# Kernel optimization log

Measured on AMD Instinct MI355X. Metric: run time of the kernel, lower is better.

The kernel has to match this reference:

```python
import jax, jax.numpy as jnp
import numpy as np

NUM_ITER = 10
NUM_LAYER = 3
EMB_DIM = 128
ALPHA = 0.1
NUM_ATOM_FEATS = 9
ATOM_VOCAB = 119
N_NODES = 50000
N_EDGES = 800000


def setup_inputs() -> dict:
    key = jax.random.key(0)
    ks = jax.random.split(key, 5)
    x = jax.random.randint(ks[0], (N_NODES, NUM_ATOM_FEATS), 0, ATOM_VOCAB, dtype=jnp.int64 if jax.config.jax_enable_x64 else jnp.int32)
    edge_index = jax.random.randint(ks[1], (2, N_EDGES), 0, N_NODES, dtype=jnp.int32)
    scale = 1.0 / np.sqrt(EMB_DIM)
    atom_emb = jax.random.normal(ks[2], (NUM_ATOM_FEATS, ATOM_VOCAB, EMB_DIM), dtype=jnp.float32) * 0.1
    Ws = jax.random.normal(ks[3], (NUM_LAYER, EMB_DIM, EMB_DIM), dtype=jnp.float32) * scale
    bs = jax.random.normal(ks[4], (NUM_LAYER, EMB_DIM), dtype=jnp.float32) * 0.01
    return {"x": x, "edge_index": edge_index, "atom_emb": atom_emb, "Ws": Ws, "bs": bs}


def _forward(x, edge_index, atom_emb, Ws, bs):
    N = x.shape[0]
    # AtomEncoder: sum of per-feature-column embeddings -> [N, d]
    h = jax.vmap(lambda tbl, ids: tbl[ids], in_axes=(0, 1))(atom_emb, x).sum(axis=0)
    # MLP stack with ReLU on all but last layer
    L = Ws.shape[0]
    for l in range(L):
        h = h @ Ws[l] + bs[l]
        if l != L - 1:
            h = jax.nn.relu(h)
    # gcn_norm with self loops, unit edge weights (eval mode: no edge dropout)
    self_idx = jnp.arange(N, dtype=edge_index.dtype)
    src = jnp.concatenate([edge_index[0], self_idx])
    dst = jnp.concatenate([edge_index[1], self_idx])
    deg = jax.ops.segment_sum(jnp.ones(src.shape[0], dtype=h.dtype), dst, num_segments=N)
    dinv = jnp.where(deg > 0, jax.lax.rsqrt(jnp.maximum(deg, 1e-12)), 0.0)
    coef = (dinv[src] * dinv[dst])[:, None]  # [E+N, 1]
    h0 = h
    def body(i, h):
        agg = jax.ops.segment_sum(coef * h[src], dst, num_segments=N)
        return (1.0 - ALPHA) * agg + ALPHA * h0
    h = jax.lax.fori_loop(0, NUM_ITER, body, h)
    return h  # JK == 'last'


def reference(x, edge_index, atom_emb, Ws, bs):
    return _forward(x, edge_index, atom_emb, Ws, bs)
```

## Files before the change

kernel.cpp:

```cpp
#include <hip/hip_runtime.h>

#define N_NODES 50000
#define NPAD    50048
#define N_EDGES 800000
#define EMB 128
#define NFEAT 9
#define VOCAB 119
#define NITER 10
#define ALPHA 0.1f

typedef __attribute__((ext_vector_type(8))) short bf16x8;
typedef __attribute__((ext_vector_type(4))) float f32x4;


__device__ inline unsigned int f2bf1(float x) {
    union { float f; unsigned u; } v; v.f = x;
    unsigned r = v.u + 0x7fffu + ((v.u >> 16) & 1u);
    return r >> 16;
}
__device__ inline unsigned int f2bf2(float lo, float hi) {
    return f2bf1(lo) | (f2bf1(hi) << 16);
}
__device__ inline float bf2f_lo(unsigned u) {
    union { unsigned u; float f; } v; v.u = u << 16; return v.f;
}
__device__ inline float bf2f_hi(unsigned u) {
    union { unsigned u; float f; } v; v.u = u & 0xffff0000u; return v.f;
}

struct __attribute__((aligned(4))) i4 { int x, y, z, w; };


__global__ void k_zero(int* __restrict__ cnt) {
    int i = blockIdx.x * blockDim.x + threadIdx.x;
    if (i < N_NODES) cnt[i] = 0;
}

__global__ void k_count(const int* __restrict__ dst, int* __restrict__ cnt,
                        int* __restrict__ ord) {
    int e = blockIdx.x * blockDim.x + threadIdx.x;
    if (e < N_EDGES) ord[e] = atomicAdd(&cnt[dst[e]], 1);
}

__global__ void k_scan1(const int* __restrict__ cnt, int* __restrict__ rowptr,
                        int* __restrict__ bsum, float* __restrict__ dinv) {
    __shared__ int s[256];
    int t = threadIdx.x;
    int idx = blockIdx.x * 256 + t;
    int v = (idx < N_NODES) ? cnt[idx] : 0;
    if (idx < N_NODES) dinv[idx] = rsqrtf((float)(v + 1));
    s[t] = v; __syncthreads();
    for (int off = 1; off < 256; off <<= 1) {
        int add = (t >= off) ? s[t - off] : 0;
        __syncthreads();
        s[t] += add;
        __syncthreads();
    }
    if (idx < N_NODES) rowptr[idx] = s[t] - v;
    if (t == 255) bsum[blockIdx.x] = s[255];
}

__global__ void k_scan2(int* __restrict__ bsum, int nb) {
    __shared__ int s[256];
    int t = threadIdx.x;
    int v = (t < nb) ? bsum[t] : 0;
    s[t] = v; __syncthreads();
    for (int off = 1; off < 256; off <<= 1) {
        int add = (t >= off) ? s[t - off] : 0;
        __syncthreads();
        s[t] += add;
        __syncthreads();
    }
    if (t < nb) bsum[t] = s[t] - v;
}

__global__ void k_scan3(int* __restrict__ rowptr, const int* __restrict__ bsum) {
    int idx = blockIdx.x * 256 + threadIdx.x;
    if (idx < N_NODES) rowptr[idx] += bsum[blockIdx.x];
}

__global__ void k_fill(const int* __restrict__ src, const int* __restrict__ dst,
                       const int* __restrict__ ord, const int* __restrict__ rowptr,
                       int* __restrict__ csr_src) {
    int e = blockIdx.x * blockDim.x + threadIdx.x;
    if (e < N_EDGES) {
        csr_src[rowptr[dst[e]] + ord[e]] = src[e];
    }
}


__global__ void k_wprep(const float* __restrict__ W, ushort* __restrict__ WT) {
    int l = blockIdx.x >> 7;
    int n = blockIdx.x & 127;
    int k = threadIdx.x;
    WT[(l * 128 + n) * 128 + k] = (ushort)f2bf1(W[(l * 128 + k) * 128 + n]);
}


__global__ void k_encode(const int* __restrict__ x, const float* __restrict__ emb,
                         unsigned* __restrict__ hb) {
    int t = threadIdx.x;
    int sub = t >> 6;
    int dq = t & 63;
    int n = blockIdx.x * 4 + sub;
    const int* xr = x + n * NFEAT;
    float s0 = 0.f, s1 = 0.f;
#pragma unroll
    for (int f = 0; f < NFEAT; ++f) {
        const float2 e = *(const float2*)&emb[(f * VOCAB + xr[f]) * EMB + 2 * dq];
        s0 += e.x; s1 += e.y;
    }
    hb[n * 64 + dq] = f2bf2(s0, s1);
}


template <int RELU, int WQ>
__global__ __launch_bounds__(256) void k_mlp_mfma(
        const uint4* __restrict__ inb,
        uint4* __restrict__ outb,
        const uint4* __restrict__ WT4,
        const float* __restrict__ bias,
        const float* __restrict__ dinv,
        float* __restrict__ h0out,
        ushort* __restrict__ q0out,
        ushort* __restrict__ h0bout) {
    int t = threadIdx.x;
    int w = t >> 6;
    int l = t & 63;
    int lr = l & 15;
    int kg = l >> 4;
    int base = blockIdx.x * 64 + w * 16;
    union U { uint4 u; bf16x8 b; };

    int arow = base + lr;
    bf16x8 afrag[4];
#pragma unroll
    for (int kc = 0; kc < 4; ++kc) {
        U cu; cu.u = inb[arow * 16 + kc * 4 + kg];
        afrag[kc] = cu.b;
    }

    f32x4 acc[8];
#pragma unroll
    for (int nt = 0; nt < 8; ++nt) {
        float bv = bias[nt * 16 + lr];
        acc[nt] = (f32x4){bv, bv, bv, bv};
    }

#pragma unroll
    for (int kc = 0; kc < 4; ++kc) {
#pragma unroll
        for (int nt = 0; nt < 8; ++nt) {
            U cu; cu.u = WT4[(nt * 16 + lr) * 16 + kc * 4 + kg];
            acc[nt] = __builtin_amdgcn_mfma_f32_16x16x32_bf16(afrag[kc], cu.b,
                                                              acc[nt], 0, 0, 0);
        }
    }

    int orow = base + kg * 4;
    float dv[4];
    if (WQ) {
#pragma unroll
        for (int r = 0; r < 4; ++r) dv[r] = dinv[orow + r];
    }
#pragma unroll
    for (int nt = 0; nt < 8; ++nt) {
        int n = nt * 16 + lr;
#pragma unroll
        for (int r = 0; r < 4; ++r) {
            float val = acc[nt][r];
            if (RELU) val = fmaxf(val, 0.f);
            if (WQ) {
                h0out[(orow + r) * 128 + n] = val;
                q0out[(orow + r) * 128 + n] = (ushort)f2bf1(val * dv[r]);
                h0bout[(orow + r) * 128 + n] = (ushort)f2bf1(val);
            } else {
                ((ushort*)outb)[(orow + r) * 128 + n] = (ushort)f2bf1(val);
            }
        }
    }
}


#define ACC8(g) \
    a0 += bf2f_lo((g).x); a1 += bf2f_hi((g).x); \
    a2 += bf2f_lo((g).y); a3 += bf2f_hi((g).y); \
    a4 += bf2f_lo((g).z); a5 += bf2f_hi((g).z); \
    a6 += bf2f_lo((g).w); a7 += bf2f_hi((g).w);

#define SEL(iv) (pair == 0 ? (iv).x : pair == 1 ? (iv).y : pair == 2 ? (iv).z : (iv).w)

template <int LAST>
__global__ __launch_bounds__(256) void k_prop(const uint4* __restrict__ qin,
                                              const float4* __restrict__ h0,
                                              const uint4* __restrict__ h0b,
                                              void* __restrict__ outb,
                                              const int* __restrict__ rowptr,
                                              const int* __restrict__ cnt,
                                              const int* __restrict__ csr_src,
                                              const float* __restrict__ dinv) {
    int t = threadIdx.x;
    int lane = t & 63;
    int pair = lane >> 4;
    int dq = lane & 15;
    int v = blockIdx.x * 4 + (t >> 6);
    int start = __builtin_amdgcn_readfirstlane(rowptr[v]);
    int c = __builtin_amdgcn_readfirstlane(cnt[v]);
    const int* cs = csr_src + start;

    float dv = dinv[v];
    uint4 qv = qin[v * 16 + dq];
    float4 hlo, hhi; uint4 hvb;
    if (LAST) {
        hlo = h0[v * 32 + 2 * dq];
        hhi = h0[v * 32 + 2 * dq + 1];
    } else {
        hvb = h0b[v * 16 + dq];
    }

    float a0 = 0.f, a1 = 0.f, a2 = 0.f, a3 = 0.f;
    float a4 = 0.f, a5 = 0.f, a6 = 0.f, a7 = 0.f;
    int i = 0;
    for (; i + 32 <= c; i += 32) {
        i4 ia = *(const i4*)(cs + i);
        i4 ib = *(const i4*)(cs + i + 4);
        i4 ic = *(const i4*)(cs + i + 8);
        i4 id = *(const i4*)(cs + i + 12);
        i4 ie = *(const i4*)(cs + i + 16);
        i4 ifq = *(const i4*)(cs + i + 20);
        i4 ig = *(const i4*)(cs + i + 24);
        i4 ih = *(const i4*)(cs + i + 28);
        int s0 = SEL(ia), s1 = SEL(ib), s2 = SEL(ic), s3 = SEL(id);
        int s4 = SEL(ie), s5 = SEL(ifq), s6 = SEL(ig), s7 = SEL(ih);
        uint4 g0 = qin[s0 * 16 + dq];
        uint4 g1 = qin[s1 * 16 + dq];
        uint4 g2 = qin[s2 * 16 + dq];
        uint4 g3 = qin[s3 * 16 + dq];
        uint4 g4 = qin[s4 * 16 + dq];
        uint4 g5 = qin[s5 * 16 + dq];
        uint4 g6 = qin[s6 * 16 + dq];
        uint4 g7 = qin[s7 * 16 + dq];
        ACC8(g0); ACC8(g1); ACC8(g2); ACC8(g3);
        ACC8(g4); ACC8(g5); ACC8(g6); ACC8(g7);
    }
    for (; i + 8 <= c; i += 8) {
        i4 ia = *(const i4*)(cs + i);
        i4 ib = *(const i4*)(cs + i + 4);
        int s0 = SEL(ia), s1 = SEL(ib);
        uint4 g0 = qin[s0 * 16 + dq];
        uint4 g1 = qin[s1 * 16 + dq];
        ACC8(g0); ACC8(g1);
    }
    for (; i < c; i += 4) {
        int e = i + pair;
        if (e < c) {
            uint4 g = qin[cs[e] * 16 + dq];
            ACC8(g);
        }
    }
    a0 += __shfl_xor(a0, 16); a0 += __shfl_xor(a0, 32);
    a1 += __shfl_xor(a1, 16); a1 += __shfl_xor(a1, 32);
    a2 += __shfl_xor(a2, 16); a2 += __shfl_xor(a2, 32);
    a3 += __shfl_xor(a3, 16); a3 += __shfl_xor(a3, 32);
    a4 += __shfl_xor(a4, 16); a4 += __shfl_xor(a4, 32);
    a5 += __shfl_xor(a5, 16); a5 += __shfl_xor(a5, 32);
    a6 += __shfl_xor(a6, 16); a6 += __shfl_xor(a6, 32);
    a7 += __shfl_xor(a7, 16); a7 += __shfl_xor(a7, 32);

    float s0 = a0 + bf2f_lo(qv.x), s1 = a1 + bf2f_hi(qv.x);
    float s2 = a2 + bf2f_lo(qv.y), s3 = a3 + bf2f_hi(qv.y);
    float s4 = a4 + bf2f_lo(qv.z), s5 = a5 + bf2f_hi(qv.z);
    float s6 = a6 + bf2f_lo(qv.w), s7 = a7 + bf2f_hi(qv.w);
    const float K = 1.f - ALPHA;

    if (LAST) {
        float h_0 = K * dv * s0 + ALPHA * hlo.x;
        float h_1 = K * dv * s1 + ALPHA * hlo.y;
        float h_2 = K * dv * s2 + ALPHA * hlo.z;
        float h_3 = K * dv * s3 + ALPHA * hlo.w;
        float h_4 = K * dv * s4 + ALPHA * hhi.x;
        float h_5 = K * dv * s5 + ALPHA * hhi.y;
        float h_6 = K * dv * s6 + ALPHA * hhi.z;
        float h_7 = K * dv * s7 + ALPHA * hhi.w;
        if (pair < 2) {
            float4 wv = (pair == 0) ? make_float4(h_0, h_1, h_2, h_3)
                                    : make_float4(h_4, h_5, h_6, h_7);
            ((float4*)outb)[v * 32 + 2 * dq + pair] = wv;
        }
    } else {
        float h_0 = K * dv * s0 + ALPHA * bf2f_lo(hvb.x);
        float h_1 = K * dv * s1 + ALPHA * bf2f_hi(hvb.x);
        float h_2 = K * dv * s2 + ALPHA * bf2f_lo(hvb.y);
        float h_3 = K * dv * s3 + ALPHA * bf2f_hi(hvb.y);
        float h_4 = K * dv * s4 + ALPHA * bf2f_lo(hvb.z);
        float h_5 = K * dv * s5 + ALPHA * bf2f_hi(hvb.z);
        float h_6 = K * dv * s6 + ALPHA * bf2f_lo(hvb.w);
        float h_7 = K * dv * s7 + ALPHA * bf2f_hi(hvb.w);
        if (pair == 0) {
            uint4 wv;
            wv.x = f2bf2(h_0 * dv, h_1 * dv);
            wv.y = f2bf2(h_2 * dv, h_3 * dv);
            wv.z = f2bf2(h_4 * dv, h_5 * dv);
            wv.w = f2bf2(h_6 * dv, h_7 * dv);
            ((uint4*)outb)[v * 16 + dq] = wv;
        }
    }
}


extern "C" void kernel_launch(void* const* d_in, const int* in_sizes, int n_in,
                              void* d_out, int out_size, void* d_ws, size_t ws_size,
                              hipStream_t stream) {
    const int*   x    = (const int*)d_in[0];
    const int*   ei   = (const int*)d_in[1];
    const float* emb  = (const float*)d_in[2];
    const float* Ws   = (const float*)d_in[3];
    const float* bs   = (const float*)d_in[4];
    float* out = (float*)d_out;

    const int* src = ei;
    const int* dst = ei + N_EDGES;

    char* w = (char*)d_ws;
    size_t off = 0;
    auto alloc = [&](size_t bytes) {
        void* p = w + off;
        off += (bytes + 255) & ~(size_t)255;
        return p;
    };
    float*  h0      = (float*)alloc((size_t)NPAD * EMB * 4);
    void*   hb      = alloc((size_t)NPAD * EMB * 2);
    void*   qA      = alloc((size_t)NPAD * EMB * 2);
    void*   qB      = alloc((size_t)NPAD * EMB * 2);
    void*   h0b     = alloc((size_t)NPAD * EMB * 2);
    ushort* WT      = (ushort*)alloc((size_t)3 * 128 * 128 * 2);
    float*  dinv    = (float*)alloc((size_t)NPAD * 4);
    int*    cnt     = (int*)alloc(N_NODES * 4);
    int*    rowptr  = (int*)alloc(N_NODES * 4);
    int*    bsum    = (int*)alloc(256 * 4);
    int*    csr_src = (int*)alloc(N_EDGES * 4);
    int*    ord     = (int*)alloc(N_EDGES * 4);
    (void)ws_size; (void)n_in; (void)in_sizes; (void)out_size;

    const int NB_N  = (N_NODES + 255) / 256;
    const int NB_E  = (N_EDGES + 255) / 256;
    const int NB_EN = N_NODES / 4;
    const int NB_M  = NPAD / 64;
    const int NB_P  = N_NODES / 4;

    k_zero<<<NB_N, 256, 0, stream>>>(cnt);
    k_count<<<NB_E, 256, 0, stream>>>(dst, cnt, ord);
    k_scan1<<<NB_N, 256, 0, stream>>>(cnt, rowptr, bsum, dinv);
    k_scan2<<<1, 256, 0, stream>>>(bsum, NB_N);
    k_scan3<<<NB_N, 256, 0, stream>>>(rowptr, bsum);
    k_fill<<<NB_E, 256, 0, stream>>>(src, dst, ord, rowptr, csr_src);

    k_wprep<<<384, 128, 0, stream>>>(Ws, WT);
    k_encode<<<NB_EN, 256, 0, stream>>>(x, emb, (unsigned*)hb);
    k_mlp_mfma<1, 0><<<NB_M, 256, 0, stream>>>(
        (const uint4*)hb, (uint4*)hb, (const uint4*)(WT + 0 * 128 * 128),
        bs + 0 * EMB, nullptr, nullptr, nullptr, nullptr);
    k_mlp_mfma<1, 0><<<NB_M, 256, 0, stream>>>(
        (const uint4*)hb, (uint4*)hb, (const uint4*)(WT + 1 * 128 * 128),
        bs + 1 * EMB, nullptr, nullptr, nullptr, nullptr);
    k_mlp_mfma<0, 1><<<NB_M, 256, 0, stream>>>(
        (const uint4*)hb, nullptr, (const uint4*)(WT + 2 * 128 * 128),
        bs + 2 * EMB, dinv, h0, (ushort*)qA, (ushort*)h0b);

    const uint4* qin = (const uint4*)qA;
    for (int i = 0; i < NITER; ++i) {
        if (i == NITER - 1) {
            k_prop<1><<<NB_P, 256, 0, stream>>>(qin, (const float4*)h0,
                                                (const uint4*)h0b, out,
                                                rowptr, cnt, csr_src, dinv);
        } else {
            void* qo = (i & 1) ? qA : qB;
            k_prop<0><<<NB_P, 256, 0, stream>>>(qin, (const float4*)h0,
                                                (const uint4*)h0b, qo,
                                                rowptr, cnt, csr_src, dinv);
            qin = (const uint4*)qo;
        }
    }
}
```

Before: 554.0 us.

## Split propagation features into column chunks and use 16-bit CSR indices

Stores the propagated bf16 features as four 32-column chunk planes, so each propagation block works on one chunk and its gather working set (about 3.2MB per chunk) is small enough to stay cache-resident. Block indices are interleaved so neighbouring blocks cover different chunks of nearby nodes. CSR source indices are packed into ushort to halve index traffic; this relies on node ids fitting in 16 bits, which 50000 does. Each wave now gathers 16 edges per step into a zero-padded dummy row instead of using unrolled tail loops, at the cost of four times more blocks and a longer shuffle reduction.

```diff
diff --git a/kernel.cpp b/kernel.cpp
--- a/kernel.cpp
+++ b/kernel.cpp
@@ -2,12 +2,14 @@
 
 #define N_NODES 50000
 #define NPAD    50048
+#define ZROW    50000
 #define N_EDGES 800000
 #define EMB 128
 #define NFEAT 9
 #define VOCAB 119
 #define NITER 10
 #define ALPHA 0.1f
+#define NCH 4
 
 typedef __attribute__((ext_vector_type(8))) short bf16x8;
 typedef __attribute__((ext_vector_type(4))) float f32x4;
@@ -27,8 +29,6 @@
 __device__ inline float bf2f_hi(unsigned u) {
     union { unsigned u; float f; } v; v.u = u & 0xffff0000u; return v.f;
 }
-
-struct __attribute__((aligned(4))) i4 { int x, y, z, w; };
 
 
 __global__ void k_zero(int* __restrict__ cnt) {
@@ -81,10 +81,21 @@
 
 __global__ void k_fill(const int* __restrict__ src, const int* __restrict__ dst,
                        const int* __restrict__ ord, const int* __restrict__ rowptr,
-                       int* __restrict__ csr_src) {
+                       ushort* __restrict__ csr_u) {
     int e = blockIdx.x * blockDim.x + threadIdx.x;
     if (e < N_EDGES) {
-        csr_src[rowptr[dst[e]] + ord[e]] = src[e];
+        csr_u[rowptr[dst[e]] + ord[e]] = (ushort)src[e];
+    }
+}
+
+__global__ void k_zpad(uint4* __restrict__ qA, uint4* __restrict__ qB) {
+    int t = threadIdx.x;
+    const uint4 z = make_uint4(0u, 0u, 0u, 0u);
+    const int per_ch = (NPAD - N_NODES) * 4;
+    for (int i = t; i < NCH * per_ch; i += 256) {
+        int ch = i / per_ch, r = i % per_ch;
+        size_t idx = (size_t)ch * NPAD * 4 + (size_t)N_NODES * 4 + r;
+        qA[idx] = z; qB[idx] = z;
     }
 }
 
@@ -172,7 +183,8 @@
             if (RELU) val = fmaxf(val, 0.f);
             if (WQ) {
                 h0out[(orow + r) * 128 + n] = val;
-                q0out[(orow + r) * 128 + n] = (ushort)f2bf1(val * dv[r]);
+                q0out[((size_t)(n >> 5) * NPAD + (orow + r)) * 32 + (n & 31)] =
+                    (ushort)f2bf1(val * dv[r]);
                 h0bout[(orow + r) * 128 + n] = (ushort)f2bf1(val);
             } else {
                 ((ushort*)outb)[(orow + r) * 128 + n] = (ushort)f2bf1(val);
@@ -188,121 +200,92 @@
     a4 += bf2f_lo((g).z); a5 += bf2f_hi((g).z); \
     a6 += bf2f_lo((g).w); a7 += bf2f_hi((g).w);
 
-#define SEL(iv) (pair == 0 ? (iv).x : pair == 1 ? (iv).y : pair == 2 ? (iv).z : (iv).w)
-
 template <int LAST>
 __global__ __launch_bounds__(256) void k_prop(const uint4* __restrict__ qin,
-                                              const float4* __restrict__ h0,
+                                              const float4* __restrict__ h0f4,
                                               const uint4* __restrict__ h0b,
                                               void* __restrict__ outb,
                                               const int* __restrict__ rowptr,
                                               const int* __restrict__ cnt,
-                                              const int* __restrict__ csr_src,
+                                              const ushort* __restrict__ csr_u,
                                               const float* __restrict__ dinv) {
     int t = threadIdx.x;
     int lane = t & 63;
-    int pair = lane >> 4;
-    int dq = lane & 15;
-    int v = blockIdx.x * 4 + (t >> 6);
+    int slot = lane >> 2;
+    int dq = lane & 3;
+    int bid = blockIdx.x;
+    int x = bid & 7;
+    int ch = x >> 1;
+    int j = bid >> 3;
+    int v = ((j << 1) + (x & 1)) * 4 + (t >> 6);
+
+    const uint4* qc = qin + (size_t)ch * NPAD * 4;
     int start = __builtin_amdgcn_readfirstlane(rowptr[v]);
     int c = __builtin_amdgcn_readfirstlane(cnt[v]);
-    const int* cs = csr_src + start;
-
+    const ushort* cs = csr_u + start;
     float dv = dinv[v];
-    uint4 qv = qin[v * 16 + dq];
-    float4 hlo, hhi; uint4 hvb;
-    if (LAST) {
-        hlo = h0[v * 32 + 2 * dq];
-        hhi = h0[v * 32 + 2 * dq + 1];
-    } else {
-        hvb = h0b[v * 16 + dq];
-    }
+    uint4 qv = qc[v * 4 + dq];
 
     float a0 = 0.f, a1 = 0.f, a2 = 0.f, a3 = 0.f;
     float a4 = 0.f, a5 = 0.f, a6 = 0.f, a7 = 0.f;
-    int i = 0;
-    for (; i + 32 <= c; i += 32) {
-        i4 ia = *(const i4*)(cs + i);
-        i4 ib = *(const i4*)(cs + i + 4);
-        i4 ic = *(const i4*)(cs + i + 8);
-        i4 id = *(const i4*)(cs + i + 12);
-        i4 ie = *(const i4*)(cs + i + 16);
-        i4 ifq = *(const i4*)(cs + i + 20);
-        i4 ig = *(const i4*)(cs + i + 24);
-        i4 ih = *(const i4*)(cs + i + 28);
-        int s0 = SEL(ia), s1 = SEL(ib), s2 = SEL(ic), s3 = SEL(id);
-        int s4 = SEL(ie), s5 = SEL(ifq), s6 = SEL(ig), s7 = SEL(ih);
-        uint4 g0 = qin[s0 * 16 + dq];
-        uint4 g1 = qin[s1 * 16 + dq];
-        uint4 g2 = qin[s2 * 16 + dq];
-        uint4 g3 = qin[s3 * 16 + dq];
-        uint4 g4 = qin[s4 * 16 + dq];
-        uint4 g5 = qin[s5 * 16 + dq];
-        uint4 g6 = qin[s6 * 16 + dq];
-        uint4 g7 = qin[s7 * 16 + dq];
-        ACC8(g0); ACC8(g1); ACC8(g2); ACC8(g3);
-        ACC8(g4); ACC8(g5); ACC8(g6); ACC8(g7);
-    }
-    for (; i + 8 <= c; i += 8) {
-        i4 ia = *(const i4*)(cs + i);
-        i4 ib = *(const i4*)(cs + i + 4);
-        int s0 = SEL(ia), s1 = SEL(ib);
-        uint4 g0 = qin[s0 * 16 + dq];
-        uint4 g1 = qin[s1 * 16 + dq];
-        ACC8(g0); ACC8(g1);
-    }
-    for (; i < c; i += 4) {
-        int e = i + pair;
-        if (e < c) {
-            uint4 g = qin[cs[e] * 16 + dq];
-            ACC8(g);
-        }
-    }
-    a0 += __shfl_xor(a0, 16); a0 += __shfl_xor(a0, 32);
-    a1 += __shfl_xor(a1, 16); a1 += __shfl_xor(a1, 32);
-    a2 += __shfl_xor(a2, 16); a2 += __shfl_xor(a2, 32);
-    a3 += __shfl_xor(a3, 16); a3 += __shfl_xor(a3, 32);
-    a4 += __shfl_xor(a4, 16); a4 += __shfl_xor(a4, 32);
-    a5 += __shfl_xor(a5, 16); a5 += __shfl_xor(a5, 32);
-    a6 += __shfl_xor(a6, 16); a6 += __shfl_xor(a6, 32);
-    a7 += __shfl_xor(a7, 16); a7 += __shfl_xor(a7, 32);
-
-    float s0 = a0 + bf2f_lo(qv.x), s1 = a1 + bf2f_hi(qv.x);
-    float s2 = a2 + bf2f_lo(qv.y), s3 = a3 + bf2f_hi(qv.y);
-    float s4 = a4 + bf2f_lo(qv.z), s5 = a5 + bf2f_hi(qv.z);
-    float s6 = a6 + bf2f_lo(qv.w), s7 = a7 + bf2f_hi(qv.w);
+
+    for (int i = 0; i < c; i += 16) {
+        int sidx = (int)__builtin_nontemporal_load(cs + i + slot);
+        int s = (i + slot < c) ? sidx : ZROW;
+        uint4 g = qc[s * 4 + dq];
+        ACC8(g);
+    }
+
+    a0 += __shfl_xor(a0, 4); a0 += __shfl_xor(a0, 8); a0 += __shfl_xor(a0, 16); a0 += __shfl_xor(a0, 32);
+    a1 += __shfl_xor(a1, 4); a1 += __shfl_xor(a1, 8); a1 += __shfl_xor(a1, 16); a1 += __shfl_xor(a1, 32);
+    a2 += __shfl_xor(a2, 4); a2 += __shfl_xor(a2, 8); a2 += __shfl_xor(a2, 16); a2 += __shfl_xor(a2, 32);
+    a3 += __shfl_xor(a3, 4); a3 += __shfl_xor(a3, 8); a3 += __shfl_xor(a3, 16); a3 += __shfl_xor(a3, 32);
+    a4 += __shfl_xor(a4, 4); a4 += __shfl_xor(a4, 8); a4 += __shfl_xor(a4, 16); a4 += __shfl_xor(a4, 32);
+    a5 += __shfl_xor(a5, 4); a5 += __shfl_xor(a5, 8); a5 += __shfl_xor(a5, 16); a5 += __shfl_xor(a5, 32);
+    a6 += __shfl_xor(a6, 4); a6 += __shfl_xor(a6, 8); a6 += __shfl_xor(a6, 16); a6 += __shfl_xor(a6, 32);
+    a7 += __shfl_xor(a7, 4); a7 += __shfl_xor(a7, 8); a7 += __shfl_xor(a7, 16); a7 += __shfl_xor(a7, 32);
+
     const float K = 1.f - ALPHA;
 
     if (LAST) {
-        float h_0 = K * dv * s0 + ALPHA * hlo.x;
-        float h_1 = K * dv * s1 + ALPHA * hlo.y;
-        float h_2 = K * dv * s2 + ALPHA * hlo.z;
-        float h_3 = K * dv * s3 + ALPHA * hlo.w;
-        float h_4 = K * dv * s4 + ALPHA * hhi.x;
-        float h_5 = K * dv * s5 + ALPHA * hhi.y;
-        float h_6 = K * dv * s6 + ALPHA * hhi.z;
-        float h_7 = K * dv * s7 + ALPHA * hhi.w;
-        if (pair < 2) {
-            float4 wv = (pair == 0) ? make_float4(h_0, h_1, h_2, h_3)
-                                    : make_float4(h_4, h_5, h_6, h_7);
-            ((float4*)outb)[v * 32 + 2 * dq + pair] = wv;
+        if (slot < 2) {
+            float4 h0v = h0f4[v * 32 + ch * 8 + dq * 2 + slot];
+            float b0, b1, b2, b3;
+            if (slot == 0) {
+                b0 = a0 + bf2f_lo(qv.x); b1 = a1 + bf2f_hi(qv.x);
+                b2 = a2 + bf2f_lo(qv.y); b3 = a3 + bf2f_hi(qv.y);
+            } else {
+                b0 = a4 + bf2f_lo(qv.z); b1 = a5 + bf2f_hi(qv.z);
+                b2 = a6 + bf2f_lo(qv.w); b3 = a7 + bf2f_hi(qv.w);
+            }
+            float4 res;
+            res.x = K * dv * b0 + ALPHA * h0v.x;
+            res.y = K * dv * b1 + ALPHA * h0v.y;
+            res.z = K * dv * b2 + ALPHA * h0v.z;
+            res.w = K * dv * b3 + ALPHA * h0v.w;
+            ((float4*)outb)[v * 32 + ch * 8 + dq * 2 + slot] = res;
         }
     } else {
-        float h_0 = K * dv * s0 + ALPHA * bf2f_lo(hvb.x);
-        float h_1 = K * dv * s1 + ALPHA * bf2f_hi(hvb.x);
-        float h_2 = K * dv * s2 + ALPHA * bf2f_lo(hvb.y);
-        float h_3 = K * dv * s3 + ALPHA * bf2f_hi(hvb.y);
-        float h_4 = K * dv * s4 + ALPHA * bf2f_lo(hvb.z);
-        float h_5 = K * dv * s5 + ALPHA * bf2f_hi(hvb.z);
-        float h_6 = K * dv * s6 + ALPHA * bf2f_lo(hvb.w);
-        float h_7 = K * dv * s7 + ALPHA * bf2f_hi(hvb.w);
-        if (pair == 0) {
+        if (slot == 0) {
+            uint4 hvb = h0b[v * 16 + ch * 4 + dq];
+            float s0 = a0 + bf2f_lo(qv.x), s1 = a1 + bf2f_hi(qv.x);
+            float s2 = a2 + bf2f_lo(qv.y), s3 = a3 + bf2f_hi(qv.y);
+            float s4 = a4 + bf2f_lo(qv.z), s5 = a5 + bf2f_hi(qv.z);
+            float s6 = a6 + bf2f_lo(qv.w), s7 = a7 + bf2f_hi(qv.w);
+            float h_0 = K * dv * s0 + ALPHA * bf2f_lo(hvb.x);
+            float h_1 = K * dv * s1 + ALPHA * bf2f_hi(hvb.x);
+            float h_2 = K * dv * s2 + ALPHA * bf2f_lo(hvb.y);
+            float h_3 = K * dv * s3 + ALPHA * bf2f_hi(hvb.y);
+            float h_4 = K * dv * s4 + ALPHA * bf2f_lo(hvb.z);
+            float h_5 = K * dv * s5 + ALPHA * bf2f_hi(hvb.z);
+            float h_6 = K * dv * s6 + ALPHA * bf2f_lo(hvb.w);
+            float h_7 = K * dv * s7 + ALPHA * bf2f_hi(hvb.w);
             uint4 wv;
             wv.x = f2bf2(h_0 * dv, h_1 * dv);
             wv.y = f2bf2(h_2 * dv, h_3 * dv);
             wv.z = f2bf2(h_4 * dv, h_5 * dv);
             wv.w = f2bf2(h_6 * dv, h_7 * dv);
-            ((uint4*)outb)[v * 16 + dq] = wv;
+            ((uint4*)outb)[(size_t)ch * NPAD * 4 + v * 4 + dq] = wv;
         }
     }
 }
@@ -330,15 +313,15 @@
     };
     float*  h0      = (float*)alloc((size_t)NPAD * EMB * 4);
     void*   hb      = alloc((size_t)NPAD * EMB * 2);
-    void*   qA      = alloc((size_t)NPAD * EMB * 2);
-    void*   qB      = alloc((size_t)NPAD * EMB * 2);
+    void*   qA      = alloc((size_t)NCH * NPAD * 32 * 2);
+    void*   qB      = alloc((size_t)NCH * NPAD * 32 * 2);
     void*   h0b     = alloc((size_t)NPAD * EMB * 2);
     ushort* WT      = (ushort*)alloc((size_t)3 * 128 * 128 * 2);
     float*  dinv    = (float*)alloc((size_t)NPAD * 4);
     int*    cnt     = (int*)alloc(N_NODES * 4);
     int*    rowptr  = (int*)alloc(N_NODES * 4);
     int*    bsum    = (int*)alloc(256 * 4);
-    int*    csr_src = (int*)alloc(N_EDGES * 4);
+    ushort* csr_u   = (ushort*)alloc((N_EDGES + 64) * 2);
     int*    ord     = (int*)alloc(N_EDGES * 4);
     (void)ws_size; (void)n_in; (void)in_sizes; (void)out_size;
 
@@ -346,14 +329,14 @@
     const int NB_E  = (N_EDGES + 255) / 256;
     const int NB_EN = N_NODES / 4;
     const int NB_M  = NPAD / 64;
-    const int NB_P  = N_NODES / 4;
+    const int NB_P  = N_NODES;
 
     k_zero<<<NB_N, 256, 0, stream>>>(cnt);
     k_count<<<NB_E, 256, 0, stream>>>(dst, cnt, ord);
     k_scan1<<<NB_N, 256, 0, stream>>>(cnt, rowptr, bsum, dinv);
     k_scan2<<<1, 256, 0, stream>>>(bsum, NB_N);
     k_scan3<<<NB_N, 256, 0, stream>>>(rowptr, bsum);
-    k_fill<<<NB_E, 256, 0, stream>>>(src, dst, ord, rowptr, csr_src);
+    k_fill<<<NB_E, 256, 0, stream>>>(src, dst, ord, rowptr, csr_u);
 
     k_wprep<<<384, 128, 0, stream>>>(Ws, WT);
     k_encode<<<NB_EN, 256, 0, stream>>>(x, emb, (unsigned*)hb);
@@ -367,17 +350,19 @@
         (const uint4*)hb, nullptr, (const uint4*)(WT + 2 * 128 * 128),
         bs + 2 * EMB, dinv, h0, (ushort*)qA, (ushort*)h0b);
 
+    k_zpad<<<1, 256, 0, stream>>>((uint4*)qA, (uint4*)qB);
+
     const uint4* qin = (const uint4*)qA;
     for (int i = 0; i < NITER; ++i) {
         if (i == NITER - 1) {
             k_prop<1><<<NB_P, 256, 0, stream>>>(qin, (const float4*)h0,
                                                 (const uint4*)h0b, out,
-                                                rowptr, cnt, csr_src, dinv);
+                                                rowptr, cnt, csr_u, dinv);
         } else {
             void* qo = (i & 1) ? qA : qB;
             k_prop<0><<<NB_P, 256, 0, stream>>>(qin, (const float4*)h0,
                                                 (const uint4*)h0b, qo,
-                                                rowptr, cnt, csr_src, dinv);
+                                                rowptr, cnt, csr_u, dinv);
             qin = (const uint4*)qo;
         }
     }
```

New measurement: 1.061 ms. 1.91x slower.
